# Performance work log

Hardware: AMD Instinct MI355X
Metric: run time of the kernel (lower is better)

Reference implementation:

```python
import jax, jax.numpy as jnp
import numpy as np


def setup_inputs() -> dict:
    key = jax.random.key(0)
    k1, k2, k3 = jax.random.split(key, 3)
    # N, C, H, W per input_specs
    x = jax.random.normal(k1, (16, 8, 1024, 1024), dtype=jnp.float32)
    # weight: (out_channels, in_channels, kH, kW)
    weight = jax.random.normal(k2, (8, 8, 3, 3), dtype=jnp.float32) * 0.1
    bias = jax.random.normal(k3, (8,), dtype=jnp.float32) * 0.1
    return {"x": x, "weight": weight, "bias": bias}


def reference(x, weight, bias):
    # DietConv2dV2's tiled per-kernel-column matmul loop is mathematically a
    # standard direct conv2d (stride=1, padding=1) followed by a bias add.
    out = jax.lax.conv_general_dilated(
        x, weight,
        window_strides=(1, 1),
        padding=((1, 1), (1, 1)),
        dimension_numbers=("NCHW", "OIHW", "NCHW"),
    )
    return out + bias[None, :, None, None]
```

## Files before the change

### kernel.cpp

```cpp
#include <hip/hip_runtime.h>
#include <hip/hip_bf16.h>


typedef __attribute__((ext_vector_type(8))) short short8;
typedef __attribute__((ext_vector_type(4))) float f32x4;

#define HH 1024
#define WW 1024
#define HWsz (1024*1024)
#define WB 64
#define HB 8
#define SROWS 10
#define UROW 72
#define FPITCH 576
#define NIT 16
#define NSITES (SROWS*UROW)

__device__ __forceinline__ int pk2(float a, float b) {
    __hip_bfloat162 h = __float22bfloat162_rn(make_float2(a, b));
    return *reinterpret_cast<int*>(&h);
}
__device__ __forceinline__ unsigned short f2bf(float f) {
    unsigned u = __float_as_uint(f);
    return (unsigned short)((u + 0x7FFFu + ((u >> 16) & 1u)) >> 16);
}
__device__ __forceinline__ void gl_lds16(const float* g, float* l) {
    __builtin_amdgcn_global_load_lds(
        (const __attribute__((address_space(1))) void*)g,
        (__attribute__((address_space(3))) void*)l, 16, 0, 0);
}

__global__ __launch_bounds__(256) void conv3x3_dma64(
    const float* __restrict__ x,
    const float* __restrict__ wgt,
    const float* __restrict__ bias,
    float* __restrict__ out)
{
    __shared__ float fplds[SROWS * FPITCH];
    __shared__ int4  bflds[NSITES];

    const int tid  = threadIdx.x;
    const int lane = tid & 63;
    const int wv   = tid >> 6;
    const int l15  = lane & 15;
    const int ch   = lane >> 4;

    const int wx    = blockIdx.x;
    const int strip = blockIdx.y;
    const int n     = blockIdx.z;
    const int w0    = wx * WB;
    const int htbase = strip * NIT * HB;

    const float* xn = x + (size_t)n * 8 * HWsz;

    const int t0  = ch;
    const int kh0 = (t0 >= 3) ? 1 : 0;
    const int kw0 = t0 - 3 * kh0;
    const int t1  = 4 + ch;
    const int kh1 = (t1 >= 6) ? 2 : 1;
    const int kw1 = t1 - 3 * kh1;
    const int off0 = kh0 * UROW + kw0 + 3;
    const int off1 = kh1 * UROW + kw1 + 3;
    const int off2 = 2 * UROW + 2 + 3;

    const int  coc = (l15 < 8) ? l15 : 7;
    const bool com = (l15 < 8);
    short8 b0, b1, b2;
    {
        const float* wp0 = wgt + coc * 72 + kh0 * 3 + kw0;
        const float* wp1 = wgt + coc * 72 + kh1 * 3 + kw1;
        const float* wp2 = wgt + coc * 72 + 2 * 3 + 2;
#pragma unroll
        for (int j = 0; j < 8; ++j) {
            b0[j] = (short)(com ? f2bf(wp0[j * 9]) : 0);
            b1[j] = (short)(com ? f2bf(wp1[j * 9]) : 0);
            b2[j] = (short)((com && ch == 0) ? f2bf(wp2[j * 9]) : 0);
        }
    }
    const float bv = com ? bias[l15] : 0.0f;

    const int sci_f = lane >> 3;
    const int swg_f = lane & 7;
    const int sci_p = lane >> 1;
    const int swg_p = lane & 1;

    auto STAGE = [&](int htile) {
        int rows[3];
        rows[0] = 2 * wv; rows[1] = 2 * wv + 1; rows[2] = 8 + wv;
        const int nr = (wv < 2) ? 3 : 2;
        for (int i = 0; i < nr; ++i) {
            const int row = rows[i];
            int gh = htile - 1 + row;
            gh = (gh < 0) ? 0 : ((gh > HH - 1) ? HH - 1 : gh);
            const float* rowf = xn + (size_t)sci_f * HWsz + (size_t)gh * WW;
#pragma unroll
            for (int q = 0; q < 2; ++q) {
                int gs = w0 - 4 + (q * 8 + swg_f) * 4;
                gs = (gs < 0) ? 0 : ((gs > WW - 4) ? WW - 4 : gs);
                gl_lds16(rowf + gs, &fplds[row * FPITCH + q * 256]);
            }
            if (lane < 16) {
                const float* rowp = xn + (size_t)sci_p * HWsz + (size_t)gh * WW;
                int gs = w0 - 4 + (16 + swg_p) * 4;
                gs = (gs > WW - 4) ? WW - 4 : gs;
                gl_lds16(rowp + gs, &fplds[row * FPITCH + 512]);
            }
        }
    };

    STAGE(htbase);

    for (int it = 0; it < NIT; ++it) {
        const int htile = htbase + it * HB;
        asm volatile("s_waitcnt vmcnt(0)" ::: "memory");
        __syncthreads();

        for (int s = tid; s < NSITES; s += 256) {
            const int row = s / UROW;
            const int u   = s - row * UROW;
            const int gh  = htile - 1 + row;
            const int gw  = w0 - 4 + u;
            const bool ok = ((unsigned)gh < (unsigned)HH) &&
                            ((unsigned)gw < (unsigned)WW);
            int fbase, cs;
            if (u < 64) {
                fbase = row * FPITCH + (u >> 5) * 256 + ((u >> 2) & 7) * 4 + (u & 3);
                cs = 32;
            } else {
                fbase = row * FPITCH + 512 + ((u >> 2) & 1) * 4 + (u & 3);
                cs = 8;
            }
            float v0 = ok ? fplds[fbase]          : 0.0f;
            float v1 = ok ? fplds[fbase + 1 * cs] : 0.0f;
            float v2 = ok ? fplds[fbase + 2 * cs] : 0.0f;
            float v3 = ok ? fplds[fbase + 3 * cs] : 0.0f;
            float v4 = ok ? fplds[fbase + 4 * cs] : 0.0f;
            float v5 = ok ? fplds[fbase + 5 * cs] : 0.0f;
            float v6 = ok ? fplds[fbase + 6 * cs] : 0.0f;
            float v7 = ok ? fplds[fbase + 7 * cs] : 0.0f;
            int4 pk;
            pk.x = pk2(v0, v1);
            pk.y = pk2(v2, v3);
            pk.z = pk2(v4, v5);
            pk.w = pk2(v6, v7);
            bflds[s] = pk;
        }
        __syncthreads();

        if (it + 1 < NIT) STAGE(htile + HB);

        f32x4 acc[2][4];
#pragma unroll
        for (int th = 0; th < 2; ++th)
#pragma unroll
            for (int wt = 0; wt < 4; ++wt) {
                acc[th][wt].x = bv; acc[th][wt].y = bv;
                acc[th][wt].z = bv; acc[th][wt].w = bv;
            }
#pragma unroll
        for (int th = 0; th < 2; ++th) {
            const int hl = wv * 2 + th;
            const int ub = hl * UROW + l15;
#pragma unroll
            for (int wt = 0; wt < 4; ++wt) {
                const int u = ub + wt * 16;
                short8 a0 = *reinterpret_cast<const short8*>(&bflds[u + off0]);
                short8 a1 = *reinterpret_cast<const short8*>(&bflds[u + off1]);
                short8 a2 = *reinterpret_cast<const short8*>(&bflds[u + off2]);
                f32x4 c = acc[th][wt];
                c = __builtin_amdgcn_mfma_f32_16x16x32_bf16(a0, b0, c, 0, 0, 0);
                c = __builtin_amdgcn_mfma_f32_16x16x32_bf16(a1, b1, c, 0, 0, 0);
                c = __builtin_amdgcn_mfma_f32_16x16x32_bf16(a2, b2, c, 0, 0, 0);
                acc[th][wt] = c;
            }
        }

        if (com) {
#pragma unroll
            for (int th = 0; th < 2; ++th) {
                const int hl = wv * 2 + th;
                float* op = out + ((size_t)n * 8 + l15) * HWsz
                                + (size_t)(htile + hl) * WW + w0 + ch * 4;
#pragma unroll
                for (int wt = 0; wt < 4; ++wt)
                    *reinterpret_cast<float4*>(op + wt * 16) =
                        *reinterpret_cast<const float4*>(&acc[th][wt]);
            }
        }
    }
}

extern "C" void kernel_launch(void* const* d_in, const int* in_sizes, int n_in,
                              void* d_out, int out_size, void* d_ws, size_t ws_size,
                              hipStream_t stream) {
    const float* x    = (const float*)d_in[0];
    const float* wgt  = (const float*)d_in[1];
    const float* bias = (const float*)d_in[2];
    float* out = (float*)d_out;

    dim3 grid(16, 8, 16);
    dim3 block(256, 1, 1);
    conv3x3_dma64<<<grid, block, 0, stream>>>(x, wgt, bias, out);
}
```

Measured before the change: 310.4 us.

## Double-buffer LDS staging to prefetch two tiles ahead and halve grid strips

Adds ping-pong LDS buffers for both the fp32 staging area and the bf16 packed tiles. The global-to-LDS DMA now runs two tiles ahead, and the bf16 conversion for the next tile runs before the MFMAs of the current one. A partial vmcnt wait lets loads stay in flight across iterations. Each block now processes twice as many row tiles and the grid has half as many strips, which amortizes the prologue but halves the number of blocks and doubles LDS use per block, lowering occupancy.

```diff
diff --git a/kernel.cpp b/kernel.cpp
--- a/kernel.cpp
+++ b/kernel.cpp
@@ -13,7 +13,7 @@
 #define SROWS 10
 #define UROW 72
 #define FPITCH 576
-#define NIT 16
+#define NIT 32
 #define NSITES (SROWS*UROW)
 
 __device__ __forceinline__ int pk2(float a, float b) {
@@ -30,14 +30,16 @@
         (__attribute__((address_space(3))) void*)l, 16, 0, 0);
 }
 
-__global__ __launch_bounds__(256) void conv3x3_dma64(
+__global__ __launch_bounds__(256) void conv3x3_pipe2(
     const float* __restrict__ x,
     const float* __restrict__ wgt,
     const float* __restrict__ bias,
     float* __restrict__ out)
 {
-    __shared__ float fplds[SROWS * FPITCH];
-    __shared__ int4  bflds[NSITES];
+    __shared__ float fpA[SROWS * FPITCH];
+    __shared__ float fpB[SROWS * FPITCH];
+    __shared__ int4  bfA[NSITES];
+    __shared__ int4  bfB[NSITES];
 
     const int tid  = threadIdx.x;
     const int lane = tid & 63;
@@ -49,7 +51,7 @@
     const int strip = blockIdx.y;
     const int n     = blockIdx.z;
     const int w0    = wx * WB;
-    const int htbase = strip * NIT * HB;
+    const int htbase = strip * (NIT * HB);
 
     const float* xn = x + (size_t)n * 8 * HWsz;
 
@@ -84,7 +86,7 @@
     const int sci_p = lane >> 1;
     const int swg_p = lane & 1;
 
-    auto STAGE = [&](int htile) {
+    auto STAGE = [&](int htile, float* fpb) {
         int rows[3];
         rows[0] = 2 * wv; rows[1] = 2 * wv + 1; rows[2] = 8 + wv;
         const int nr = (wv < 2) ? 3 : 2;
@@ -97,24 +99,18 @@
             for (int q = 0; q < 2; ++q) {
                 int gs = w0 - 4 + (q * 8 + swg_f) * 4;
                 gs = (gs < 0) ? 0 : ((gs > WW - 4) ? WW - 4 : gs);
-                gl_lds16(rowf + gs, &fplds[row * FPITCH + q * 256]);
-            }
-            if (lane < 16) {
+                gl_lds16(rowf + gs, &fpb[row * FPITCH + q * 256]);
+            }
+            {
                 const float* rowp = xn + (size_t)sci_p * HWsz + (size_t)gh * WW;
                 int gs = w0 - 4 + (16 + swg_p) * 4;
                 gs = (gs > WW - 4) ? WW - 4 : gs;
-                gl_lds16(rowp + gs, &fplds[row * FPITCH + 512]);
+                if (lane < 16) gl_lds16(rowp + gs, &fpb[row * FPITCH + 512]);
             }
         }
     };
 
-    STAGE(htbase);
-
-    for (int it = 0; it < NIT; ++it) {
-        const int htile = htbase + it * HB;
-        asm volatile("s_waitcnt vmcnt(0)" ::: "memory");
-        __syncthreads();
-
+    auto TRANS = [&](int htile, const float* fpb, int4* bfb) {
         for (int s = tid; s < NSITES; s += 256) {
             const int row = s / UROW;
             const int u   = s - row * UROW;
@@ -130,25 +126,55 @@
                 fbase = row * FPITCH + 512 + ((u >> 2) & 1) * 4 + (u & 3);
                 cs = 8;
             }
-            float v0 = ok ? fplds[fbase]          : 0.0f;
-            float v1 = ok ? fplds[fbase + 1 * cs] : 0.0f;
-            float v2 = ok ? fplds[fbase + 2 * cs] : 0.0f;
-            float v3 = ok ? fplds[fbase + 3 * cs] : 0.0f;
-            float v4 = ok ? fplds[fbase + 4 * cs] : 0.0f;
-            float v5 = ok ? fplds[fbase + 5 * cs] : 0.0f;
-            float v6 = ok ? fplds[fbase + 6 * cs] : 0.0f;
-            float v7 = ok ? fplds[fbase + 7 * cs] : 0.0f;
+            float v0 = ok ? fpb[fbase]          : 0.0f;
+            float v1 = ok ? fpb[fbase + 1 * cs] : 0.0f;
+            float v2 = ok ? fpb[fbase + 2 * cs] : 0.0f;
+            float v3 = ok ? fpb[fbase + 3 * cs] : 0.0f;
+            float v4 = ok ? fpb[fbase + 4 * cs] : 0.0f;
+            float v5 = ok ? fpb[fbase + 5 * cs] : 0.0f;
+            float v6 = ok ? fpb[fbase + 6 * cs] : 0.0f;
+            float v7 = ok ? fpb[fbase + 7 * cs] : 0.0f;
             int4 pk;
             pk.x = pk2(v0, v1);
             pk.y = pk2(v2, v3);
             pk.z = pk2(v4, v5);
             pk.w = pk2(v6, v7);
-            bflds[s] = pk;
-        }
-        __syncthreads();
-
-        if (it + 1 < NIT) STAGE(htile + HB);
-
+            bfb[s] = pk;
+        }
+    };
+
+    STAGE(htbase, fpA);
+    STAGE(htbase + HB, fpB);
+    asm volatile("s_waitcnt vmcnt(0)" ::: "memory");
+    __builtin_amdgcn_sched_barrier(0);
+    __builtin_amdgcn_s_barrier();
+    TRANS(htbase, fpA, bfA);
+    asm volatile("s_waitcnt lgkmcnt(0)" ::: "memory");
+    __builtin_amdgcn_sched_barrier(0);
+    __builtin_amdgcn_s_barrier();
+
+    for (int k = 0; k < NIT; ++k) {
+        const int htile = htbase + k * HB;
+
+        asm volatile("s_waitcnt vmcnt(8)" ::: "memory");
+        __builtin_amdgcn_sched_barrier(0);
+        __builtin_amdgcn_s_barrier();
+
+        {
+            const float* fsrc = ((k + 1) & 1) ? fpB : fpA;
+            int4*        bdst = ((k + 1) & 1) ? bfB : bfA;
+            TRANS(htile + HB, fsrc, bdst);
+        }
+        asm volatile("s_waitcnt lgkmcnt(0)" ::: "memory");
+        __builtin_amdgcn_sched_barrier(0);
+        __builtin_amdgcn_s_barrier();
+
+        {
+            int t2 = k + 2; if (t2 > NIT - 1) t2 = NIT - 1;
+            STAGE(htbase + t2 * HB, (k & 1) ? fpB : fpA);
+        }
+
+        const int4* bsrc = (k & 1) ? bfB : bfA;
         f32x4 acc[2][4];
 #pragma unroll
         for (int th = 0; th < 2; ++th)
@@ -164,9 +190,9 @@
 #pragma unroll
             for (int wt = 0; wt < 4; ++wt) {
                 const int u = ub + wt * 16;
-                short8 a0 = *reinterpret_cast<const short8*>(&bflds[u + off0]);
-                short8 a1 = *reinterpret_cast<const short8*>(&bflds[u + off1]);
-                short8 a2 = *reinterpret_cast<const short8*>(&bflds[u + off2]);
+                short8 a0 = *reinterpret_cast<const short8*>(&bsrc[u + off0]);
+                short8 a1 = *reinterpret_cast<const short8*>(&bsrc[u + off1]);
+                short8 a2 = *reinterpret_cast<const short8*>(&bsrc[u + off2]);
                 f32x4 c = acc[th][wt];
                 c = __builtin_amdgcn_mfma_f32_16x16x32_bf16(a0, b0, c, 0, 0, 0);
                 c = __builtin_amdgcn_mfma_f32_16x16x32_bf16(a1, b1, c, 0, 0, 0);
@@ -174,7 +200,6 @@
                 acc[th][wt] = c;
             }
         }
-
         if (com) {
 #pragma unroll
             for (int th = 0; th < 2; ++th) {
@@ -198,7 +223,7 @@
     const float* bias = (const float*)d_in[2];
     float* out = (float*)d_out;
 
-    dim3 grid(16, 8, 16);
+    dim3 grid(16, 4, 16);
     dim3 block(256, 1, 1);
-    conv3x3_dma64<<<grid, block, 0, stream>>>(x, wgt, bias, out);
-}
+    conv3x3_pipe2<<<grid, block, 0, stream>>>(x, wgt, bias, out);
+}
```

After: 333.3 us. 1.07x slower.
